# Performance work log

Measured on AMD Instinct MI355X. Metric: run time of the kernel, lower is better.

## Reference

```python
import jax, jax.numpy as jnp
import numpy as np

N_HEADS = 16
MAX_LEN = 4096
D_MODEL = 1024
EPS = 1e-6


def setup_inputs() -> dict:
    key = jax.random.key(0)
    ks = jax.random.split(key, 12)
    B, L, D = 4, 4096, D_MODEL
    s = 1.0 / np.sqrt(D)
    inp = {
        "q": jax.random.normal(ks[0], (B, L, D), jnp.float32),
        "k": jax.random.normal(ks[1], (B, L, D), jnp.float32),
        "v": jax.random.normal(ks[2], (B, L, D), jnp.float32),
        "Wq": jax.random.normal(ks[3], (D, D), jnp.float32) * s,
        "bq": jax.random.normal(ks[4], (D,), jnp.float32) * s,
        "Wk": jax.random.normal(ks[5], (D, D), jnp.float32) * s,
        "bk": jax.random.normal(ks[6], (D,), jnp.float32) * s,
        "Wv": jax.random.normal(ks[7], (D, D), jnp.float32) * s,
        "bv": jax.random.normal(ks[8], (D,), jnp.float32) * s,
        "Wo": jax.random.normal(ks[9], (D, D), jnp.float32) * s,
        "bo": jax.random.normal(ks[10], (D,), jnp.float32) * s,
    }
    return inp


def _cos_attn(q, k, v, Wq, bq, Wk, bk, Wv, bv, Wo, bo):
    B, Lq, D = q.shape
    Lk = k.shape[1]
    H = N_HEADS
    hd = D // H
    # torch Linear: x @ W^T + b
    qh = (q @ Wq.T + bq).reshape(B, Lq, H, hd).transpose(0, 2, 1, 3)  # b h l d
    kh = (k @ Wk.T + bk).reshape(B, Lk, H, hd).transpose(0, 2, 1, 3)
    vh = (v @ Wv.T + bv).reshape(B, Lk, H, hd).transpose(0, 2, 1, 3)
    qh = jax.nn.relu(qh)
    kh = jax.nn.relu(kh)
    # weight_index buffer: pi*(1..max_len)/(2*max_len), shape (1,1,L,1)
    idx = (np.pi * jnp.arange(1, MAX_LEN + 1, dtype=jnp.float32) / (2 * MAX_LEN))
    qi = idx[:Lq][None, None, :, None]
    ki = idx[:Lk][None, None, :, None]
    q_ = jnp.concatenate([qh * jnp.sin(qi), qh * jnp.cos(qi)], axis=-1)  # b h l 2d
    k_ = jnp.concatenate([kh * jnp.sin(ki), kh * jnp.cos(ki)], axis=-1)
    kv_ = jnp.einsum("bnld,bnlm->bndm", k_, vh)  # b h 2d d
    z_ = 1.0 / jnp.maximum(jnp.einsum("bnld,bnd->bnl", q_, jnp.sum(k_, axis=2)), EPS)
    attn = jnp.einsum("bnld,bndm,bnl->bnlm", q_, kv_, z_)  # b h l d
    attn = attn.transpose(0, 2, 1, 3).reshape(B, Lq, D)
    return attn @ Wo.T + bo  # dropout: eval mode (identity)


def reference(q, k, v, Wq, bq, Wk, bk, Wv, bv, Wo, bo):
    return _cos_attn(q, k, v, Wq, bq, Wk, bk, Wv, bv, Wo, bo)
```

## Files before the change

### kernel.cpp

```cpp
#include <hip/hip_runtime.h>

typedef __bf16 bf16x8 __attribute__((ext_vector_type(8)));
typedef float f32x4 __attribute__((ext_vector_type(4)));

#define PI_F 3.14159265358979323846f

__device__ __forceinline__ unsigned short f2bf(float f) {
  unsigned u = __builtin_bit_cast(unsigned, f);
  u += 0x7fffu + ((u >> 16) & 1u);
  return (unsigned short)(u >> 16);
}

__device__ __forceinline__ unsigned scale_pair(unsigned w, float f) {
  const float lo = __builtin_bit_cast(float, w << 16);
  const float hi = __builtin_bit_cast(float, w & 0xffff0000u);
  return (unsigned)f2bf(lo * f) | ((unsigned)f2bf(hi * f) << 16);
}

#define GLD16(gp, lp)                                          \
  __builtin_amdgcn_global_load_lds(                            \
      (const __attribute__((address_space(1))) void*)(gp),     \
      (__attribute__((address_space(3))) void*)(lp), 16, 0, 0)

struct AReg { float4 a0, a1, a2, a3, a4, a5, a6, a7; };

__device__ __forceinline__ uint4 cvtpk16(float4 x, float4 y) {
  unsigned c0, c1, c2, c3;
  asm("v_cvt_pk_bf16_f32 %0, %1, %2" : "=v"(c0) : "v"(x.x), "v"(x.y));
  asm("v_cvt_pk_bf16_f32 %0, %1, %2" : "=v"(c1) : "v"(x.z), "v"(x.w));
  asm("v_cvt_pk_bf16_f32 %0, %1, %2" : "=v"(c2) : "v"(y.x), "v"(y.y));
  asm("v_cvt_pk_bf16_f32 %0, %1, %2" : "=v"(c3) : "v"(y.z), "v"(y.w));
  uint4 u; u.x = c0; u.y = c1; u.z = c2; u.w = c3;
  return u;
}

__device__ __forceinline__ uint2 cvtpk8(float a, float b, float c, float d) {
  unsigned lo, hi;
  asm("v_cvt_pk_bf16_f32 %0, %1, %2" : "=v"(lo) : "v"(a), "v"(b));
  asm("v_cvt_pk_bf16_f32 %0, %1, %2" : "=v"(hi) : "v"(c), "v"(d));
  uint2 r; r.x = lo; r.y = hi;
  return r;
}

__device__ __forceinline__ void unpack8(uint4 w, float* f) {
  f[0] = __builtin_bit_cast(float, w.x << 16);
  f[1] = __builtin_bit_cast(float, w.x & 0xffff0000u);
  f[2] = __builtin_bit_cast(float, w.y << 16);
  f[3] = __builtin_bit_cast(float, w.y & 0xffff0000u);
  f[4] = __builtin_bit_cast(float, w.z << 16);
  f[5] = __builtin_bit_cast(float, w.z & 0xffff0000u);
  f[6] = __builtin_bit_cast(float, w.w << 16);
  f[7] = __builtin_bit_cast(float, w.w & 0xffff0000u);
}

__global__ __launch_bounds__(256) void convert_w(
    const float* __restrict__ Wq, const float* __restrict__ Wk,
    const float* __restrict__ Wv, const float* __restrict__ Wo,
    unsigned short* __restrict__ Wqb, unsigned short* __restrict__ Wkb,
    unsigned short* __restrict__ Wvb, unsigned short* __restrict__ Wob) {
  const int region = blockIdx.y;
  const float* s; unsigned short* d;
  switch (region) {
    case 0: s = Wq; d = Wqb; break;
    case 1: s = Wk; d = Wkb; break;
    case 2: s = Wv; d = Wvb; break;
    default: s = Wo; d = Wob; break;
  }
  const float4* s4 = (const float4*)s;
  ushort4* d4 = (ushort4*)d;
  const int n4 = 262144;
  for (int i = blockIdx.x * 256 + threadIdx.x; i < n4; i += gridDim.x * 256) {
    float4 f = s4[i];
    ushort4 o;
    o.x = f2bf(f.x); o.y = f2bf(f.y); o.z = f2bf(f.z); o.w = f2bf(f.w);
    d4[i] = o;
  }
}

template <int MODE, bool AF32>
__global__ __launch_bounds__(512, 2) void gemm256(
    const void* __restrict__ Ain, const unsigned short* __restrict__ Bw,
    const float* __restrict__ bias, void* __restrict__ out) {
  constexpr int K = 1024, NKT = 16;
  __shared__ unsigned short S[65536];
  const int tid = threadIdx.x;
  const int wave = tid >> 6, lane = tid & 63;
  const int fr = lane & 15, fq = lane >> 4;
  const int wr = wave >> 2, wc = wave & 3;
  const int cpx = gridDim.x >> 3;
  const int wg = (blockIdx.x & 7) * cpx + (blockIdx.x >> 3);
  const int mt = wg >> 2, ntile = wg & 3;
  const int m0 = mt * 256, n0 = ntile * 256;

  const int srow = tid >> 3;
  const int ac16 = tid & 7;
  const int scolE = ((ac16 << 4) ^ ((srow & 7) << 4)) >> 1;
  const unsigned short* bSrc = Bw + (size_t)(n0 + srow) * K + scolE;
  const unsigned short* aSrcB =
      AF32 ? (const unsigned short*)nullptr
           : ((const unsigned short*)Ain + (size_t)(m0 + srow) * K + scolE);
  const float* A32 = (const float*)Ain;
  const int awoff = (ac16 ^ (srow & 7)) << 3;
  AReg R;

#define BSTAGE(kt_, buf_) do {                                                     \
    const int kc_ = (kt_) * 64;                                                    \
    GLD16(bSrc + kc_,                  S + (buf_) * 32768 + 16384 + wave * 512);   \
    GLD16(bSrc + (size_t)65536 + kc_,  S + (buf_) * 32768 + 20480 + wave * 512);   \
    GLD16(bSrc + (size_t)131072 + kc_, S + (buf_) * 32768 + 24576 + wave * 512);   \
    GLD16(bSrc + (size_t)196608 + kc_, S + (buf_) * 32768 + 28672 + wave * 512);   \
  } while (0)

#define ASTAGE(kt_, buf_) do {                                                     \
    const int kc_ = (kt_) * 64;                                                    \
    GLD16(aSrcB + kc_,                  S + (buf_) * 32768 +     0 + wave * 512);  \
    GLD16(aSrcB + (size_t)65536 + kc_,  S + (buf_) * 32768 +  4096 + wave * 512);  \
    GLD16(aSrcB + (size_t)131072 + kc_, S + (buf_) * 32768 +  8192 + wave * 512);  \
    GLD16(aSrcB + (size_t)196608 + kc_, S + (buf_) * 32768 + 12288 + wave * 512);  \
  } while (0)

#define ALOAD_ALL(kt_) do {                                                        \
    const int kc_ = (kt_) * 64;                                                    \
    const float4* p_;                                                              \
    p_ = (const float4*)(A32 + (size_t)(m0 + srow) * K + kc_) + ac16 * 2;          \
    R.a0 = p_[0]; R.a1 = p_[1];                                                    \
    p_ = (const float4*)(A32 + (size_t)(m0 + 64 + srow) * K + kc_) + ac16 * 2;     \
    R.a2 = p_[0]; R.a3 = p_[1];                                                    \
    p_ = (const float4*)(A32 + (size_t)(m0 + 128 + srow) * K + kc_) + ac16 * 2;    \
    R.a4 = p_[0]; R.a5 = p_[1];                                                    \
    p_ = (const float4*)(A32 + (size_t)(m0 + 192 + srow) * K + kc_) + ac16 * 2;    \
    R.a6 = p_[0]; R.a7 = p_[1];                                                    \
  } while (0)

#define AWRITE_ALL(buf_) do {                                                      \
    unsigned short* dst_ = &S[(buf_) * 32768 + srow * 64 + awoff];                 \
    *(uint4*)(dst_)         = cvtpk16(R.a0, R.a1);                                 \
    *(uint4*)(dst_ + 4096)  = cvtpk16(R.a2, R.a3);                                 \
    *(uint4*)(dst_ + 8192)  = cvtpk16(R.a4, R.a5);                                 \
    *(uint4*)(dst_ + 12288) = cvtpk16(R.a6, R.a7);                                 \
  } while (0)

  const int xorv = (fr & 7) << 4;
  const unsigned cbE0 = (unsigned)(((fq * 16) ^ xorv) >> 1);
  const unsigned cbE1 = (unsigned)(((64 + fq * 16) ^ xorv) >> 1);

  f32x4 acc[8][4] = {};
  if constexpr (AF32) {
    ALOAD_ALL(0);
    BSTAGE(0, 0);
    AWRITE_ALL(0);
  } else {
    BSTAGE(0, 0);
    ASTAGE(0, 0);
  }
  asm volatile("s_waitcnt vmcnt(0) lgkmcnt(0)" ::: "memory");
  __syncthreads();

  for (int kt = 0; kt < NKT; ++kt) {
    const int buf = kt & 1;
    const unsigned aB = (unsigned)(buf * 32768 + wr * 8192 + fr * 64);
    const unsigned bB = (unsigned)(buf * 32768 + 16384 + (wc >> 1) * 8192 +
                                   ((wc & 1) * 64 + fr) * 64);
#pragma unroll
    for (int ph = 0; ph < 4; ++ph) {
      const int mh = ph >> 1, nh = ph & 1;
      bf16x8 af[4][2], bfr[2][2];
#pragma unroll
      for (int mm = 0; mm < 4; ++mm) {
        const unsigned r = aB + (unsigned)((mh * 4 + mm) * 1024);
        af[mm][0] = *(const bf16x8*)&S[r + cbE0];
        af[mm][1] = *(const bf16x8*)&S[r + cbE1];
      }
#pragma unroll
      for (int nn = 0; nn < 2; ++nn) {
        const unsigned r = bB + (unsigned)((nh * 2 + nn) * 1024);
        bfr[nn][0] = *(const bf16x8*)&S[r + cbE0];
        bfr[nn][1] = *(const bf16x8*)&S[r + cbE1];
      }
      if (ph == 0 && kt + 1 < NKT) {
        if constexpr (AF32) ALOAD_ALL(kt + 1);
        BSTAGE(kt + 1, buf ^ 1);
        if constexpr (!AF32) ASTAGE(kt + 1, buf ^ 1);
      }
      if constexpr (AF32) {
        if (ph == 2 && kt + 1 < NKT) AWRITE_ALL(buf ^ 1);
      }
      __builtin_amdgcn_s_barrier();
      __builtin_amdgcn_s_setprio(1);
#pragma unroll
      for (int mm = 0; mm < 4; ++mm)
#pragma unroll
        for (int nn = 0; nn < 2; ++nn) {
          acc[mh * 4 + mm][nh * 2 + nn] = __builtin_amdgcn_mfma_f32_16x16x32_bf16(
              af[mm][0], bfr[nn][0], acc[mh * 4 + mm][nh * 2 + nn], 0, 0, 0);
          acc[mh * 4 + mm][nh * 2 + nn] = __builtin_amdgcn_mfma_f32_16x16x32_bf16(
              af[mm][1], bfr[nn][1], acc[mh * 4 + mm][nh * 2 + nn], 0, 0, 0);
        }
      __builtin_amdgcn_s_setprio(0);
      if (ph == 3) {
        if constexpr (AF32) {
          asm volatile("s_waitcnt lgkmcnt(0)" ::: "memory");
          __builtin_amdgcn_sched_barrier(0);
        }
        asm volatile("s_waitcnt vmcnt(0)" ::: "memory");
      }
      __builtin_amdgcn_s_barrier();
    }
  }
#undef BSTAGE
#undef ASTAGE
#undef ALOAD_ALL
#undef AWRITE_ALL

  const int rowb = m0 + wr * 128 + fq * 4;
  const int colb = n0 + wc * 64 + fr;
  const int rtb0 = wr * 128 + fq * 4;
  const int mlo = m0 & 4095;
  const int b16 = (m0 >> 12) << 4;
  const int hbase = n0 >> 6;

  if constexpr (MODE == 0) {
#pragma unroll
    for (int nq = 0; nq < 4; ++nq) {
      const int col = colb + nq * 16;
      const float bb = bias[col];
      const int h = col >> 6, dd = col & 63;
#pragma unroll
      for (int mq = 0; mq < 8; ++mq) {
#pragma unroll
        for (int rr = 0; rr < 4; ++rr) {
          const int i = rowb + mq * 16 + rr;
          const int b = i >> 12, l = i & 4095;
          const float val = fmaxf(acc[mq][nq][rr] + bb, 0.0f);
          ((unsigned short*)out)[((size_t)((b << 4) + h) * 4096 + l) * 64 + dd] = f2bf(val);
        }
      }
    }
  } else if constexpr (MODE == 2) {
    float* Sf = (float*)S;
    float* O = (float*)out;
    float bb4[4];
#pragma unroll
    for (int nq = 0; nq < 4; ++nq) bb4[nq] = bias[colb + nq * 16];
    const int colL = wc * 64;
#pragma unroll
    for (int h4 = 0; h4 < 4; ++h4) {
      __syncthreads();
      if (wr == (h4 >> 1)) {
        const int mqb = (h4 & 1) * 4;
#pragma unroll
        for (int mq2 = 0; mq2 < 4; ++mq2) {
          const int rl = mq2 * 16 + fq * 4;
#pragma unroll
          for (int nq = 0; nq < 4; ++nq) {
#pragma unroll
            for (int rr = 0; rr < 4; ++rr)
              Sf[(rl + rr) * 260 + colL + nq * 16 + fr] = acc[mqb + mq2][nq][rr] + bb4[nq];
          }
        }
      }
      __syncthreads();
#pragma unroll
      for (int i = 0; i < 8; ++i) {
        const int rl = wave * 8 + i;
        const int gr = m0 + h4 * 64 + rl;
        f32x4 v4 = *(const f32x4*)&Sf[rl * 260 + lane * 4];
        __builtin_nontemporal_store(v4, (f32x4*)(O + (size_t)gr * 1024 + n0 + lane * 4));
      }
    }
  } else {
    float bb4[4];
#pragma unroll
    for (int nq = 0; nq < 4; ++nq) bb4[nq] = bias[colb + nq * 16];
#pragma unroll
    for (int mq = 0; mq < 8; ++mq)
#pragma unroll
      for (int nq = 0; nq < 4; ++nq)
#pragma unroll
        for (int rr = 0; rr < 4; ++rr) {
          float val = acc[mq][nq][rr] + bb4[nq];
          if constexpr (MODE == 5) val = fmaxf(val, 0.0f);
          acc[mq][nq][rr] = val;
        }
    unsigned short* G = (unsigned short*)out;
    __syncthreads();
#pragma unroll
    for (int mq = 0; mq < 8; ++mq) {
      const int rtb = rtb0 + mq * 16;
#pragma unroll
      for (int nq = 0; nq < 4; ++nq) {
        const int ct = wc * 64 + nq * 16 + fr;
        uint2 w = cvtpk8(acc[mq][nq][0], acc[mq][nq][1], acc[mq][nq][2], acc[mq][nq][3]);
        *(uint2*)&S[ct * 256 + (rtb ^ ((ct & 7) << 2))] = w;
      }
    }
    __syncthreads();
#pragma unroll
    for (int it = 0; it < 16; ++it) {
      const int ct = it * 16 + (tid >> 5);
      const int lo = (tid & 31) << 3;
      const int sw = (ct & 7) << 2;
      uint2 r0 = *(const uint2*)&S[ct * 256 + (lo ^ sw)];
      uint2 r1 = *(const uint2*)&S[ct * 256 + ((lo + 4) ^ sw)];
      uint4 w; w.x = r0.x; w.y = r0.y; w.z = r1.x; w.w = r1.y;
      const int h = hbase + (ct >> 6), dd = ct & 63;
      const size_t addr = ((size_t)(b16 + h) * 64 + dd) * 4096 + mlo + lo;
      *(uint4*)(G + addr) = w;
    }
  }
}

__global__ __launch_bounds__(256, 2) void kv_gemm(
    const unsigned short* __restrict__ Vt,
    const unsigned short* __restrict__ Kt,
    float* __restrict__ kvp) {
  __shared__ unsigned short As[64 * 64];
  __shared__ unsigned short Bs[128 * 64];
  __shared__ float sn[512], cn[512];
  const int tid = threadIdx.x, wave = tid >> 6, lane = tid & 63;
  const int fr = lane & 15, fq = lane >> 4;
  const int ls = blockIdx.x, bh = blockIdx.y;
  const size_t base = (size_t)bh * 64 * 4096;
  {
    float s0, c0, s1, c1;
    __sincosf(PI_F * (float)(ls * 512 + tid + 1) * (1.0f / 8192.0f), &s0, &c0);
    __sincosf(PI_F * (float)(ls * 512 + tid + 257) * (1.0f / 8192.0f), &s1, &c1);
    sn[tid] = s0; cn[tid] = c0;
    sn[tid + 256] = s1; cn[tid + 256] = c1;
  }
  f32x4 acc[5][2] = {};
  bf16x8 ones;
#pragma unroll
  for (int j = 0; j < 8; ++j) ones[j] = (__bf16)1.0f;
  for (int t = 0; t < 8; ++t) {
    const int l0 = ls * 512 + t * 64;
    __syncthreads();
#pragma unroll
    for (int j = 0; j < 2; ++j) {
      const int p = j * 256 + tid;
      const int row = p >> 3, cc = (p & 7) ^ (row & 7);
      GLD16(Vt + base + (size_t)row * 4096 + l0 + cc * 8,
            As + ((j << 8) + (wave << 6)) * 8);
    }
#pragma unroll
    for (int j = 0; j < 2; ++j) {
      const int p = j * 256 + tid;
      const int kr = p >> 3, cc = p & 7;
      const uint4 w = *(const uint4*)(Kt + base + (size_t)kr * 4096 + l0 + cc * 8);
      const int tl = t * 64 + cc * 8;
      float kf[8];
      unpack8(w, kf);
      const float4 sA = *(const float4*)&sn[tl], sB = *(const float4*)&sn[tl + 4];
      const float4 cA = *(const float4*)&cn[tl], cB = *(const float4*)&cn[tl + 4];
      float4 x0, x1;
      x0.x = kf[0] * sA.x; x0.y = kf[1] * sA.y; x0.z = kf[2] * sA.z; x0.w = kf[3] * sA.w;
      x1.x = kf[4] * sB.x; x1.y = kf[5] * sB.y; x1.z = kf[6] * sB.z; x1.w = kf[7] * sB.w;
      const uint4 wsn = cvtpk16(x0, x1);
      x0.x = kf[0] * cA.x; x0.y = kf[1] * cA.y; x0.z = kf[2] * cA.z; x0.w = kf[3] * cA.w;
      x1.x = kf[4] * cB.x; x1.y = kf[5] * cB.y; x1.z = kf[6] * cB.z; x1.w = kf[7] * cB.w;
      const uint4 wcn = cvtpk16(x0, x1);
      const int sw_ = cc ^ (kr & 7);
      *(uint4*)&Bs[(kr * 8 + sw_) * 8] = wsn;
      *(uint4*)&Bs[((kr + 64) * 8 + sw_) * 8] = wcn;
    }
    __syncthreads();
#pragma unroll
    for (int kk = 0; kk < 2; ++kk) {
      const int ch = kk * 4 + fq;
      bf16x8 a[4], b[2];
#pragma unroll
      for (int m = 0; m < 4; ++m) {
        const int r = m * 16 + fr;
        a[m] = *(const bf16x8*)&As[(r * 8 + (ch ^ (r & 7))) * 8];
      }
#pragma unroll
      for (int n = 0; n < 2; ++n) {
        const int r = wave * 32 + n * 16 + fr;
        b[n] = *(const bf16x8*)&Bs[(r * 8 + (ch ^ (r & 7))) * 8];
      }
#pragma unroll
      for (int m = 0; m < 4; ++m)
#pragma unroll
        for (int n = 0; n < 2; ++n)
          acc[m][n] = __builtin_amdgcn_mfma_f32_16x16x32_bf16(a[m], b[n], acc[m][n], 0, 0, 0);
#pragma unroll
      for (int n = 0; n < 2; ++n)
        acc[4][n] = __builtin_amdgcn_mfma_f32_16x16x32_bf16(ones, b[n], acc[4][n], 0, 0, 0);
    }
  }
  float* outp = kvp + ((size_t)bh * 8 + ls) * (65 * 128);
  const int colb = wave * 32 + fr;
#pragma unroll
  for (int n = 0; n < 2; ++n) {
    const int col = colb + n * 16;
#pragma unroll
    for (int m = 0; m < 4; ++m)
#pragma unroll
      for (int r = 0; r < 4; ++r)
        outp[(m * 16 + fq * 4 + r) * 128 + col] = acc[m][n][r];
    if (fq == 0) outp[64 * 128 + col] = acc[4][n][0];
  }
}

__global__ __launch_bounds__(256) void kv_reduce(
    const float* __restrict__ kvp, unsigned short* __restrict__ kv_ext) {
  const int bh = blockIdx.x;
  for (int e = threadIdx.x; e < 80 * 128; e += 256) {
    const int row = e >> 7, c = e & 127;
    float v = 0.0f;
    if (row < 65) {
#pragma unroll
      for (int ls = 0; ls < 8; ++ls)
        v += kvp[((size_t)bh * 8 + ls) * (65 * 128) + row * 128 + c];
    }
    kv_ext[(size_t)bh * (80 * 128) + e] = f2bf(v);
  }
}

__global__ __launch_bounds__(256) void attn_phase2(
    const unsigned short* __restrict__ Qh, const unsigned short* __restrict__ kve,
    unsigned short* __restrict__ attn) {
  __shared__ unsigned short Qs[128 * 128];
  __shared__ unsigned short Ws[80 * 128];
  const int tid = threadIdx.x, wave = tid >> 6, lane = tid & 63;
  const int fr = lane & 15, fq = lane >> 4;
  const int l0 = blockIdx.x * 128;
  const int bh = blockIdx.y, b = bh >> 4, h = bh & 15;
#pragma unroll
  for (int j = 0; j < 5; ++j) {
    const int p = j * 256 + tid;
    const int r = p >> 4, scn = p & 15;
    const int cc = scn ^ (r & 7);
    GLD16(kve + ((size_t)bh * 80 + r) * 128 + cc * 8,
          Ws + ((size_t)(j * 256 + wave * 64)) * 8);
  }
#pragma unroll
  for (int it = 0; it < 4; ++it) {
    const int qc = it * 256 + tid;
    const int r = qc >> 3, dc = qc & 7;
    const uint4 w = *(const uint4*)(Qh + ((size_t)bh * 4096 + l0 + r) * 64 + dc * 8);
    float sv, cv;
    __sincosf(PI_F * (float)(l0 + r + 1) * (1.0f / 8192.0f), &sv, &cv);
    uint4 osn, ocs;
    osn.x = scale_pair(w.x, sv); osn.y = scale_pair(w.y, sv);
    osn.z = scale_pair(w.z, sv); osn.w = scale_pair(w.w, sv);
    ocs.x = scale_pair(w.x, cv); ocs.y = scale_pair(w.y, cv);
    ocs.z = scale_pair(w.z, cv); ocs.w = scale_pair(w.w, cv);
    const int ps = r * 16 + (dc ^ (r & 7));
    *(uint4*)&Qs[ps * 8] = osn;
    *(uint4*)&Qs[(ps + 8) * 8] = ocs;
  }
  __syncthreads();
  f32x4 acc[2][5] = {};
#pragma unroll
  for (int kk = 0; kk < 4; ++kk) {
    const int cc = kk * 4 + fq;
    bf16x8 a[2], bb[5];
#pragma unroll
    for (int m = 0; m < 2; ++m) {
      const int r = wave * 32 + m * 16 + fr;
      a[m] = *(const bf16x8*)&Qs[(r * 16 + (cc ^ (r & 7))) * 8];
    }
#pragma unroll
    for (int n = 0; n < 5; ++n) {
      const int r = n * 16 + fr;
      bb[n] = *(const bf16x8*)&Ws[(r * 16 + (cc ^ (r & 7))) * 8];
    }
#pragma unroll
    for (int m = 0; m < 2; ++m)
#pragma unroll
      for (int n = 0; n < 5; ++n)
        acc[m][n] = __builtin_amdgcn_mfma_f32_16x16x32_bf16(a[m], bb[n], acc[m][n], 0, 0, 0);
  }
#pragma unroll
  for (int m = 0; m < 2; ++m) {
#pragma unroll
    for (int r = 0; r < 4; ++r) {
      const float den = __shfl(acc[m][4][r], lane & 48);
      const float z = 1.0f / fmaxf(den, 1e-6f);
      const int l = l0 + wave * 32 + m * 16 + fq * 4 + r;
      const size_t ro = ((size_t)b * 4096 + l) * 1024 + (size_t)h * 64;
#pragma unroll
      for (int n = 0; n < 4; ++n)
        attn[ro + n * 16 + fr] = f2bf(acc[m][n][r] * z);
    }
  }
}

extern "C" void kernel_launch(void* const* d_in, const int* in_sizes, int n_in,
                              void* d_out, int out_size, void* d_ws, size_t ws_size,
                              hipStream_t stream) {
  (void)in_sizes; (void)n_in; (void)out_size; (void)ws_size;
  const float* q  = (const float*)d_in[0];
  const float* k  = (const float*)d_in[1];
  const float* v  = (const float*)d_in[2];
  const float* Wq = (const float*)d_in[3];
  const float* bq = (const float*)d_in[4];
  const float* Wk = (const float*)d_in[5];
  const float* bk = (const float*)d_in[6];
  const float* Wv = (const float*)d_in[7];
  const float* bvp = (const float*)d_in[8];
  const float* Wo = (const float*)d_in[9];
  const float* bo = (const float*)d_in[10];

  char* ws = (char*)d_ws;
  unsigned short* Wqb = (unsigned short*)(ws + 0);
  unsigned short* Wkb = (unsigned short*)(ws + 2097152);
  unsigned short* Wvb = (unsigned short*)(ws + 4194304);
  unsigned short* Wob = (unsigned short*)(ws + 6291456);
  unsigned short* Qh  = (unsigned short*)(ws + 8388608);
  unsigned short* Vt  = (unsigned short*)(ws + 41943040);
  unsigned short* Kt  = (unsigned short*)(ws + 75497472);
  unsigned short* attnb = Kt;
  float* kvp          = (float*)(ws + 109051904);
  unsigned short* kve = (unsigned short*)(ws + 126091264);

  convert_w<<<dim3(128, 4), 256, 0, stream>>>(Wq, Wk, Wv, Wo, Wqb, Wkb, Wvb, Wob);
  gemm256<0, true><<<256, 512, 0, stream>>>(q, Wqb, bq, Qh);
  gemm256<5, true><<<256, 512, 0, stream>>>(k, Wkb, bk, Kt);
  gemm256<4, true><<<256, 512, 0, stream>>>(v, Wvb, bvp, Vt);
  kv_gemm<<<dim3(8, 64), 256, 0, stream>>>(Vt, Kt, kvp);
  kv_reduce<<<64, 256, 0, stream>>>(kvp, kve);
  attn_phase2<<<dim3(32, 64), 256, 0, stream>>>(Qh, kve, attnb);
  gemm256<2, false><<<256, 512, 0, stream>>>(attnb, Wob, bo, (float*)d_out);
}
```

Baseline: 279.8 us.

## Restructure GEMM main loop from four phases into two with B fragment reuse

Replaces the four-phase inner k-step (each reloading A and B fragments from LDS) with two halves. B fragments are loaded once per k-tile and reused across both M halves, which halves the barriers per tile and cuts LDS reads of B. The final output store also switches from a nontemporal store to a regular store. Holding both B halves raises register pressure, and the change alters how prefetch and LDS writes interleave with the MFMA work.

```diff
diff --git a/kernel.cpp b/kernel.cpp
--- a/kernel.cpp
+++ b/kernel.cpp
@@ -161,51 +161,69 @@
     const unsigned aB = (unsigned)(buf * 32768 + wr * 8192 + fr * 64);
     const unsigned bB = (unsigned)(buf * 32768 + 16384 + (wc >> 1) * 8192 +
                                    ((wc & 1) * 64 + fr) * 64);
-#pragma unroll
-    for (int ph = 0; ph < 4; ++ph) {
-      const int mh = ph >> 1, nh = ph & 1;
-      bf16x8 af[4][2], bfr[2][2];
-#pragma unroll
-      for (int mm = 0; mm < 4; ++mm) {
-        const unsigned r = aB + (unsigned)((mh * 4 + mm) * 1024);
-        af[mm][0] = *(const bf16x8*)&S[r + cbE0];
-        af[mm][1] = *(const bf16x8*)&S[r + cbE1];
-      }
+    bf16x8 af[4][2], b0[2][2], b1[2][2];
+#pragma unroll
+    for (int mm = 0; mm < 4; ++mm) {
+      const unsigned r = aB + (unsigned)(mm * 1024);
+      af[mm][0] = *(const bf16x8*)&S[r + cbE0];
+      af[mm][1] = *(const bf16x8*)&S[r + cbE1];
+    }
+#pragma unroll
+    for (int nn = 0; nn < 2; ++nn) {
+      const unsigned r0 = bB + (unsigned)(nn * 1024);
+      b0[nn][0] = *(const bf16x8*)&S[r0 + cbE0];
+      b0[nn][1] = *(const bf16x8*)&S[r0 + cbE1];
+      const unsigned r1 = bB + (unsigned)((2 + nn) * 1024);
+      b1[nn][0] = *(const bf16x8*)&S[r1 + cbE0];
+      b1[nn][1] = *(const bf16x8*)&S[r1 + cbE1];
+    }
+    if (kt + 1 < NKT) {
+      if constexpr (AF32) {
+        ALOAD_ALL(kt + 1);
+        BSTAGE(kt + 1, buf ^ 1);
+      } else {
+        BSTAGE(kt + 1, buf ^ 1);
+        ASTAGE(kt + 1, buf ^ 1);
+      }
+    }
+    __builtin_amdgcn_s_barrier();
+    __builtin_amdgcn_s_setprio(1);
+#pragma unroll
+    for (int mm = 0; mm < 4; ++mm) {
 #pragma unroll
       for (int nn = 0; nn < 2; ++nn) {
-        const unsigned r = bB + (unsigned)((nh * 2 + nn) * 1024);
-        bfr[nn][0] = *(const bf16x8*)&S[r + cbE0];
-        bfr[nn][1] = *(const bf16x8*)&S[r + cbE1];
-      }
-      if (ph == 0 && kt + 1 < NKT) {
-        if constexpr (AF32) ALOAD_ALL(kt + 1);
-        BSTAGE(kt + 1, buf ^ 1);
-        if constexpr (!AF32) ASTAGE(kt + 1, buf ^ 1);
-      }
-      if constexpr (AF32) {
-        if (ph == 2 && kt + 1 < NKT) AWRITE_ALL(buf ^ 1);
-      }
-      __builtin_amdgcn_s_barrier();
-      __builtin_amdgcn_s_setprio(1);
-#pragma unroll
-      for (int mm = 0; mm < 4; ++mm)
-#pragma unroll
-        for (int nn = 0; nn < 2; ++nn) {
-          acc[mh * 4 + mm][nh * 2 + nn] = __builtin_amdgcn_mfma_f32_16x16x32_bf16(
-              af[mm][0], bfr[nn][0], acc[mh * 4 + mm][nh * 2 + nn], 0, 0, 0);
-          acc[mh * 4 + mm][nh * 2 + nn] = __builtin_amdgcn_mfma_f32_16x16x32_bf16(
-              af[mm][1], bfr[nn][1], acc[mh * 4 + mm][nh * 2 + nn], 0, 0, 0);
-        }
-      __builtin_amdgcn_s_setprio(0);
-      if (ph == 3) {
-        if constexpr (AF32) {
-          asm volatile("s_waitcnt lgkmcnt(0)" ::: "memory");
-          __builtin_amdgcn_sched_barrier(0);
-        }
-        asm volatile("s_waitcnt vmcnt(0)" ::: "memory");
-      }
-      __builtin_amdgcn_s_barrier();
-    }
+        acc[mm][nn] = __builtin_amdgcn_mfma_f32_16x16x32_bf16(af[mm][0], b0[nn][0], acc[mm][nn], 0, 0, 0);
+        acc[mm][nn] = __builtin_amdgcn_mfma_f32_16x16x32_bf16(af[mm][1], b0[nn][1], acc[mm][nn], 0, 0, 0);
+        acc[mm][2 + nn] = __builtin_amdgcn_mfma_f32_16x16x32_bf16(af[mm][0], b1[nn][0], acc[mm][2 + nn], 0, 0, 0);
+        acc[mm][2 + nn] = __builtin_amdgcn_mfma_f32_16x16x32_bf16(af[mm][1], b1[nn][1], acc[mm][2 + nn], 0, 0, 0);
+      }
+    }
+    __builtin_amdgcn_s_setprio(0);
+    __builtin_amdgcn_s_barrier();
+#pragma unroll
+    for (int mm = 0; mm < 4; ++mm) {
+      const unsigned r = aB + (unsigned)((4 + mm) * 1024);
+      af[mm][0] = *(const bf16x8*)&S[r + cbE0];
+      af[mm][1] = *(const bf16x8*)&S[r + cbE1];
+    }
+    if constexpr (AF32) {
+      if (kt + 1 < NKT) AWRITE_ALL(buf ^ 1);
+    }
+    __builtin_amdgcn_s_barrier();
+    __builtin_amdgcn_s_setprio(1);
+#pragma unroll
+    for (int mm = 0; mm < 4; ++mm) {
+#pragma unroll
+      for (int nn = 0; nn < 2; ++nn) {
+        acc[4 + mm][nn] = __builtin_amdgcn_mfma_f32_16x16x32_bf16(af[mm][0], b0[nn][0], acc[4 + mm][nn], 0, 0, 0);
+        acc[4 + mm][nn] = __builtin_amdgcn_mfma_f32_16x16x32_bf16(af[mm][1], b0[nn][1], acc[4 + mm][nn], 0, 0, 0);
+        acc[4 + mm][2 + nn] = __builtin_amdgcn_mfma_f32_16x16x32_bf16(af[mm][0], b1[nn][0], acc[4 + mm][2 + nn], 0, 0, 0);
+        acc[4 + mm][2 + nn] = __builtin_amdgcn_mfma_f32_16x16x32_bf16(af[mm][1], b1[nn][1], acc[4 + mm][2 + nn], 0, 0, 0);
+      }
+    }
+    __builtin_amdgcn_s_setprio(0);
+    asm volatile("s_waitcnt vmcnt(0) lgkmcnt(0)" ::: "memory");
+    __builtin_amdgcn_s_barrier();
   }
 #undef BSTAGE
 #undef ASTAGE
@@ -265,7 +283,7 @@
         const int rl = wave * 8 + i;
         const int gr = m0 + h4 * 64 + rl;
         f32x4 v4 = *(const f32x4*)&Sf[rl * 260 + lane * 4];
-        __builtin_nontemporal_store(v4, (f32x4*)(O + (size_t)gr * 1024 + n0 + lane * 4));
+        *(f32x4*)(O + (size_t)gr * 1024 + n0 + lane * 4) = v4;
       }
     }
   } else {
```

Result: faster. 262.5 us (-6.2%).

## Shrink projection GEMM tiles to 128x128 with 4-deep B-operand pipeline

Applied to the files above, without the earlier changes.

Replaces the 256x256-tile, 512-thread GEMM with a 128x128-tile, 256-thread kernel using K-step 32 and a 4-stage LDS ring for async global-to-LDS loads. The grid grows from 256 to 1024 blocks, which fills more CUs on a 256-CU part and cuts shared memory per block so more blocks can be resident. The epilogues are reworked for the smaller tile. In exchange, arithmetic intensity per tile drops, each input is re-read from global memory more often, and there are more barriers per unit of work.

```diff
diff --git a/kernel.cpp b/kernel.cpp
--- a/kernel.cpp
+++ b/kernel.cpp
@@ -21,8 +21,6 @@
   __builtin_amdgcn_global_load_lds(                            \
       (const __attribute__((address_space(1))) void*)(gp),     \
       (__attribute__((address_space(3))) void*)(lp), 16, 0, 0)
-
-struct AReg { float4 a0, a1, a2, a3, a4, a5, a6, a7; };
 
 __device__ __forceinline__ uint4 cvtpk16(float4 x, float4 y) {
   unsigned c0, c1, c2, c3;
@@ -78,143 +76,127 @@
 }
 
 template <int MODE, bool AF32>
-__global__ __launch_bounds__(512, 2) void gemm256(
+__global__ __launch_bounds__(256, AF32 ? 3 : 2) void gemm128(
     const void* __restrict__ Ain, const unsigned short* __restrict__ Bw,
     const float* __restrict__ bias, void* __restrict__ out) {
-  constexpr int K = 1024, NKT = 16;
-  __shared__ unsigned short S[65536];
+  constexpr int K = 1024, NKT = 32;
+  __shared__ unsigned short S[AF32 ? 24576 : 32768];
+  constexpr int BOFF = AF32 ? 8192 : 16384;
   const int tid = threadIdx.x;
   const int wave = tid >> 6, lane = tid & 63;
   const int fr = lane & 15, fq = lane >> 4;
-  const int wr = wave >> 2, wc = wave & 3;
-  const int cpx = gridDim.x >> 3;
-  const int wg = (blockIdx.x & 7) * cpx + (blockIdx.x >> 3);
-  const int mt = wg >> 2, ntile = wg & 3;
-  const int m0 = mt * 256, n0 = ntile * 256;
-
-  const int srow = tid >> 3;
-  const int ac16 = tid & 7;
-  const int scolE = ((ac16 << 4) ^ ((srow & 7) << 4)) >> 1;
-  const unsigned short* bSrc = Bw + (size_t)(n0 + srow) * K + scolE;
-  const unsigned short* aSrcB =
+  const int wr = wave >> 1, wc = wave & 1;
+  const int wg = (blockIdx.x & 7) * 128 + (blockIdx.x >> 3);
+  const int mt = wg >> 3, nt = wg & 7;
+  const int m0 = mt * 128, n0 = nt * 128;
+
+  const int crow = tid >> 2, cq = tid & 3;
+  const int colE = ((cq ^ ((crow >> 1) & 3)) << 3);
+  const unsigned short* bSrc0 = Bw + (size_t)(n0 + crow) * K + colE;
+  const unsigned short* bSrc1 = bSrc0 + (size_t)64 * K;
+  const unsigned short* aSrc0 =
       AF32 ? (const unsigned short*)nullptr
-           : ((const unsigned short*)Ain + (size_t)(m0 + srow) * K + scolE);
+           : ((const unsigned short*)Ain + (size_t)(m0 + crow) * K + colE);
+  const unsigned short* aSrc1 = AF32 ? (const unsigned short*)nullptr : aSrc0 + (size_t)64 * K;
   const float* A32 = (const float*)Ain;
-  const int awoff = (ac16 ^ (srow & 7)) << 3;
-  AReg R;
-
-#define BSTAGE(kt_, buf_) do {                                                     \
-    const int kc_ = (kt_) * 64;                                                    \
-    GLD16(bSrc + kc_,                  S + (buf_) * 32768 + 16384 + wave * 512);   \
-    GLD16(bSrc + (size_t)65536 + kc_,  S + (buf_) * 32768 + 20480 + wave * 512);   \
-    GLD16(bSrc + (size_t)131072 + kc_, S + (buf_) * 32768 + 24576 + wave * 512);   \
-    GLD16(bSrc + (size_t)196608 + kc_, S + (buf_) * 32768 + 28672 + wave * 512);   \
+  const int arow = tid >> 1, ah = tid & 1;
+  const int ac0 = (((ah * 2) ^ ((arow >> 1) & 3)) << 3);
+  const int ac1 = (((ah * 2 + 1) ^ ((arow >> 1) & 3)) << 3);
+  const float* aSrc32_0 = A32 + (size_t)(m0 + arow) * K + ac0;
+  const float* aSrc32_1 = A32 + (size_t)(m0 + arow) * K + ac1;
+  float4 R0, R1, R2, R3;
+
+#define BSTAGE(kt_) do {                                                        \
+    const int kc_ = (kt_) * 32, bo_ = BOFF + ((kt_) & 3) * 4096;                \
+    GLD16(bSrc0 + kc_, S + bo_ + wave * 512);                                   \
+    GLD16(bSrc1 + kc_, S + bo_ + 2048 + wave * 512);                            \
   } while (0)
 
-#define ASTAGE(kt_, buf_) do {                                                     \
-    const int kc_ = (kt_) * 64;                                                    \
-    GLD16(aSrcB + kc_,                  S + (buf_) * 32768 +     0 + wave * 512);  \
-    GLD16(aSrcB + (size_t)65536 + kc_,  S + (buf_) * 32768 +  4096 + wave * 512);  \
-    GLD16(aSrcB + (size_t)131072 + kc_, S + (buf_) * 32768 +  8192 + wave * 512);  \
-    GLD16(aSrcB + (size_t)196608 + kc_, S + (buf_) * 32768 + 12288 + wave * 512);  \
+#define ASTAGE(kt_) do {                                                        \
+    const int kc_ = (kt_) * 32, ao_ = ((kt_) & 3) * 4096;                       \
+    GLD16(aSrc0 + kc_, S + ao_ + wave * 512);                                   \
+    GLD16(aSrc1 + kc_, S + ao_ + 2048 + wave * 512);                            \
   } while (0)
 
-#define ALOAD_ALL(kt_) do {                                                        \
-    const int kc_ = (kt_) * 64;                                                    \
-    const float4* p_;                                                              \
-    p_ = (const float4*)(A32 + (size_t)(m0 + srow) * K + kc_) + ac16 * 2;          \
-    R.a0 = p_[0]; R.a1 = p_[1];                                                    \
-    p_ = (const float4*)(A32 + (size_t)(m0 + 64 + srow) * K + kc_) + ac16 * 2;     \
-    R.a2 = p_[0]; R.a3 = p_[1];                                                    \
-    p_ = (const float4*)(A32 + (size_t)(m0 + 128 + srow) * K + kc_) + ac16 * 2;    \
-    R.a4 = p_[0]; R.a5 = p_[1];                                                    \
-    p_ = (const float4*)(A32 + (size_t)(m0 + 192 + srow) * K + kc_) + ac16 * 2;    \
-    R.a6 = p_[0]; R.a7 = p_[1];                                                    \
+#define ALOAD(kt_) do {                                                         \
+    const int kc_ = (kt_) * 32;                                                 \
+    R0 = *(const float4*)(aSrc32_0 + kc_);                                      \
+    R1 = *(const float4*)(aSrc32_0 + kc_ + 4);                                  \
+    R2 = *(const float4*)(aSrc32_1 + kc_);                                      \
+    R3 = *(const float4*)(aSrc32_1 + kc_ + 4);                                  \
   } while (0)
 
-#define AWRITE_ALL(buf_) do {                                                      \
-    unsigned short* dst_ = &S[(buf_) * 32768 + srow * 64 + awoff];                 \
-    *(uint4*)(dst_)         = cvtpk16(R.a0, R.a1);                                 \
-    *(uint4*)(dst_ + 4096)  = cvtpk16(R.a2, R.a3);                                 \
-    *(uint4*)(dst_ + 8192)  = cvtpk16(R.a4, R.a5);                                 \
-    *(uint4*)(dst_ + 12288) = cvtpk16(R.a6, R.a7);                                 \
+#define AWRITE(kt_) do {                                                        \
+    unsigned short* d_ = &S[((kt_) & 1) * 4096 + arow * 32];                    \
+    *(uint4*)(d_ + ah * 16)     = cvtpk16(R0, R1);                              \
+    *(uint4*)(d_ + ah * 16 + 8) = cvtpk16(R2, R3);                              \
   } while (0)
 
-  const int xorv = (fr & 7) << 4;
-  const unsigned cbE0 = (unsigned)(((fq * 16) ^ xorv) >> 1);
-  const unsigned cbE1 = (unsigned)(((64 + fq * 16) ^ xorv) >> 1);
-
-  f32x4 acc[8][4] = {};
+  const unsigned fcol = (unsigned)((fq ^ ((fr >> 1) & 3)) << 3);
+
+  f32x4 acc[4][4] = {};
   if constexpr (AF32) {
-    ALOAD_ALL(0);
-    BSTAGE(0, 0);
-    AWRITE_ALL(0);
+    BSTAGE(0);
+    ALOAD(0);
+    BSTAGE(1);
+    BSTAGE(2);
+    AWRITE(0);
+    asm volatile("s_waitcnt lgkmcnt(0)" ::: "memory");
+    __syncthreads();
   } else {
-    BSTAGE(0, 0);
-    ASTAGE(0, 0);
-  }
-  asm volatile("s_waitcnt vmcnt(0) lgkmcnt(0)" ::: "memory");
-  __syncthreads();
+    ASTAGE(0); BSTAGE(0);
+    ASTAGE(1); BSTAGE(1);
+    ASTAGE(2); BSTAGE(2);
+    asm volatile("s_waitcnt vmcnt(8)" ::: "memory");
+    __syncthreads();
+  }
 
   for (int kt = 0; kt < NKT; ++kt) {
-    const int buf = kt & 1;
-    const unsigned aB = (unsigned)(buf * 32768 + wr * 8192 + fr * 64);
-    const unsigned bB = (unsigned)(buf * 32768 + 16384 + (wc >> 1) * 8192 +
-                                   ((wc & 1) * 64 + fr) * 64);
-#pragma unroll
-    for (int ph = 0; ph < 4; ++ph) {
-      const int mh = ph >> 1, nh = ph & 1;
-      bf16x8 af[4][2], bfr[2][2];
-#pragma unroll
-      for (int mm = 0; mm < 4; ++mm) {
-        const unsigned r = aB + (unsigned)((mh * 4 + mm) * 1024);
-        af[mm][0] = *(const bf16x8*)&S[r + cbE0];
-        af[mm][1] = *(const bf16x8*)&S[r + cbE1];
-      }
-#pragma unroll
-      for (int nn = 0; nn < 2; ++nn) {
-        const unsigned r = bB + (unsigned)((nh * 2 + nn) * 1024);
-        bfr[nn][0] = *(const bf16x8*)&S[r + cbE0];
-        bfr[nn][1] = *(const bf16x8*)&S[r + cbE1];
-      }
-      if (ph == 0 && kt + 1 < NKT) {
-        if constexpr (AF32) ALOAD_ALL(kt + 1);
-        BSTAGE(kt + 1, buf ^ 1);
-        if constexpr (!AF32) ASTAGE(kt + 1, buf ^ 1);
-      }
-      if constexpr (AF32) {
-        if (ph == 2 && kt + 1 < NKT) AWRITE_ALL(buf ^ 1);
-      }
-      __builtin_amdgcn_s_barrier();
-      __builtin_amdgcn_s_setprio(1);
-#pragma unroll
-      for (int mm = 0; mm < 4; ++mm)
-#pragma unroll
-        for (int nn = 0; nn < 2; ++nn) {
-          acc[mh * 4 + mm][nh * 2 + nn] = __builtin_amdgcn_mfma_f32_16x16x32_bf16(
-              af[mm][0], bfr[nn][0], acc[mh * 4 + mm][nh * 2 + nn], 0, 0, 0);
-          acc[mh * 4 + mm][nh * 2 + nn] = __builtin_amdgcn_mfma_f32_16x16x32_bf16(
-              af[mm][1], bfr[nn][1], acc[mh * 4 + mm][nh * 2 + nn], 0, 0, 0);
-        }
-      __builtin_amdgcn_s_setprio(0);
-      if (ph == 3) {
-        if constexpr (AF32) {
-          asm volatile("s_waitcnt lgkmcnt(0)" ::: "memory");
-          __builtin_amdgcn_sched_barrier(0);
-        }
+    const unsigned abuf = (unsigned)((AF32 ? (kt & 1) : (kt & 3)) * 4096);
+    const unsigned bbuf = (unsigned)(BOFF + (kt & 3) * 4096);
+    bf16x8 a[4], b[4];
+#pragma unroll
+    for (int m = 0; m < 4; ++m) {
+      const unsigned row = (unsigned)(wr * 64 + m * 16 + fr);
+      a[m] = *(const bf16x8*)&S[abuf + row * 32 + fcol];
+    }
+#pragma unroll
+    for (int n = 0; n < 4; ++n) {
+      const unsigned row = (unsigned)(wc * 64 + n * 16 + fr);
+      b[n] = *(const bf16x8*)&S[bbuf + row * 32 + fcol];
+    }
+    if constexpr (AF32) {
+      if (kt + 1 < NKT) ALOAD(kt + 1);
+      if (kt + 3 < NKT) BSTAGE(kt + 3);
+    } else {
+      if (kt + 3 < NKT) { ASTAGE(kt + 3); BSTAGE(kt + 3); }
+    }
+    __builtin_amdgcn_s_setprio(1);
+#pragma unroll
+    for (int m = 0; m < 4; ++m)
+#pragma unroll
+      for (int n = 0; n < 4; ++n)
+        acc[m][n] = __builtin_amdgcn_mfma_f32_16x16x32_bf16(a[m], b[n], acc[m][n], 0, 0, 0);
+    __builtin_amdgcn_s_setprio(0);
+    if constexpr (AF32) {
+      if (kt + 1 < NKT) AWRITE(kt + 1);
+      asm volatile("s_waitcnt lgkmcnt(0)" ::: "memory");
+    } else {
+      if (kt < NKT - 3) {
+        asm volatile("s_waitcnt vmcnt(8)" ::: "memory");
+      } else {
         asm volatile("s_waitcnt vmcnt(0)" ::: "memory");
       }
-      __builtin_amdgcn_s_barrier();
-    }
+    }
+    __builtin_amdgcn_s_barrier();
   }
 #undef BSTAGE
 #undef ASTAGE
-#undef ALOAD_ALL
-#undef AWRITE_ALL
-
-  const int rowb = m0 + wr * 128 + fq * 4;
+#undef ALOAD
+#undef AWRITE
+
+  const int rowb = m0 + wr * 64 + fq * 4;
   const int colb = n0 + wc * 64 + fr;
-  const int rtb0 = wr * 128 + fq * 4;
   const int mlo = m0 & 4095;
   const int b16 = (m0 >> 12) << 4;
   const int hbase = n0 >> 6;
@@ -226,7 +208,7 @@
       const float bb = bias[col];
       const int h = col >> 6, dd = col & 63;
 #pragma unroll
-      for (int mq = 0; mq < 8; ++mq) {
+      for (int mq = 0; mq < 4; ++mq) {
 #pragma unroll
         for (int rr = 0; rr < 4; ++rr) {
           const int i = rowb + mq * 16 + rr;
@@ -242,30 +224,29 @@
     float bb4[4];
 #pragma unroll
     for (int nq = 0; nq < 4; ++nq) bb4[nq] = bias[colb + nq * 16];
-    const int colL = wc * 64;
-#pragma unroll
-    for (int h4 = 0; h4 < 4; ++h4) {
+#pragma unroll
+    for (int p = 0; p < 2; ++p) {
       __syncthreads();
-      if (wr == (h4 >> 1)) {
-        const int mqb = (h4 & 1) * 4;
-#pragma unroll
-        for (int mq2 = 0; mq2 < 4; ++mq2) {
-          const int rl = mq2 * 16 + fq * 4;
+      if (wr == p) {
+#pragma unroll
+        for (int mq = 0; mq < 4; ++mq) {
 #pragma unroll
           for (int nq = 0; nq < 4; ++nq) {
 #pragma unroll
-            for (int rr = 0; rr < 4; ++rr)
-              Sf[(rl + rr) * 260 + colL + nq * 16 + fr] = acc[mqb + mq2][nq][rr] + bb4[nq];
+            for (int rr = 0; rr < 4; ++rr) {
+              const int rl = mq * 16 + fq * 4 + rr;
+              Sf[rl * 132 + wc * 64 + nq * 16 + fr] = acc[mq][nq][rr] + bb4[nq];
+            }
           }
         }
       }
       __syncthreads();
 #pragma unroll
-      for (int i = 0; i < 8; ++i) {
-        const int rl = wave * 8 + i;
-        const int gr = m0 + h4 * 64 + rl;
-        f32x4 v4 = *(const f32x4*)&Sf[rl * 260 + lane * 4];
-        __builtin_nontemporal_store(v4, (f32x4*)(O + (size_t)gr * 1024 + n0 + lane * 4));
+      for (int it = 0; it < 8; ++it) {
+        const int rl = it * 8 + (tid >> 5);
+        const int col = (tid & 31) << 2;
+        f32x4 v4 = *(const f32x4*)&Sf[rl * 132 + col];
+        *(f32x4*)(O + (size_t)(m0 + p * 64 + rl) * 1024 + n0 + col) = v4;
       }
     }
   } else {
@@ -273,7 +254,7 @@
 #pragma unroll
     for (int nq = 0; nq < 4; ++nq) bb4[nq] = bias[colb + nq * 16];
 #pragma unroll
-    for (int mq = 0; mq < 8; ++mq)
+    for (int mq = 0; mq < 4; ++mq)
 #pragma unroll
       for (int nq = 0; nq < 4; ++nq)
 #pragma unroll
@@ -283,29 +264,34 @@
           acc[mq][nq][rr] = val;
         }
     unsigned short* G = (unsigned short*)out;
-    __syncthreads();
-#pragma unroll
-    for (int mq = 0; mq < 8; ++mq) {
-      const int rtb = rtb0 + mq * 16;
-#pragma unroll
-      for (int nq = 0; nq < 4; ++nq) {
-        const int ct = wc * 64 + nq * 16 + fr;
-        uint2 w = cvtpk8(acc[mq][nq][0], acc[mq][nq][1], acc[mq][nq][2], acc[mq][nq][3]);
-        *(uint2*)&S[ct * 256 + (rtb ^ ((ct & 7) << 2))] = w;
-      }
-    }
-    __syncthreads();
-#pragma unroll
-    for (int it = 0; it < 16; ++it) {
-      const int ct = it * 16 + (tid >> 5);
-      const int lo = (tid & 31) << 3;
-      const int sw = (ct & 7) << 2;
-      uint2 r0 = *(const uint2*)&S[ct * 256 + (lo ^ sw)];
-      uint2 r1 = *(const uint2*)&S[ct * 256 + ((lo + 4) ^ sw)];
-      uint4 w; w.x = r0.x; w.y = r0.y; w.z = r1.x; w.w = r1.y;
-      const int h = hbase + (ct >> 6), dd = ct & 63;
-      const size_t addr = ((size_t)(b16 + h) * 64 + dd) * 4096 + mlo + lo;
-      *(uint4*)(G + addr) = w;
+    const int rtb0 = wr * 64 + fq * 4;
+#pragma unroll
+    for (int p = 0; p < 2; ++p) {
+      __syncthreads();
+      if (wc == p) {
+#pragma unroll
+        for (int mq = 0; mq < 4; ++mq) {
+          const int rtb = rtb0 + mq * 16;
+#pragma unroll
+          for (int nq = 0; nq < 4; ++nq) {
+            const int ctl = nq * 16 + fr;
+            uint2 w = cvtpk8(acc[mq][nq][0], acc[mq][nq][1], acc[mq][nq][2], acc[mq][nq][3]);
+            *(uint2*)&S[ctl * 128 + (rtb ^ ((ctl & 7) << 2))] = w;
+          }
+        }
+      }
+      __syncthreads();
+#pragma unroll
+      for (int it = 0; it < 4; ++it) {
+        const int ctl = it * 16 + (tid >> 4);
+        const int lo = (tid & 15) << 3;
+        const int sw = (ctl & 7) << 2;
+        uint2 r0 = *(const uint2*)&S[ctl * 128 + (lo ^ sw)];
+        uint2 r1 = *(const uint2*)&S[ctl * 128 + ((lo + 4) ^ sw)];
+        uint4 w; w.x = r0.x; w.y = r0.y; w.z = r1.x; w.w = r1.y;
+        const size_t addr = ((size_t)(b16 + hbase + p) * 64 + ctl) * 4096 + mlo + lo;
+        *(uint4*)(G + addr) = w;
+      }
     }
   }
 }
@@ -516,11 +502,11 @@
   unsigned short* kve = (unsigned short*)(ws + 126091264);
 
   convert_w<<<dim3(128, 4), 256, 0, stream>>>(Wq, Wk, Wv, Wo, Wqb, Wkb, Wvb, Wob);
-  gemm256<0, true><<<256, 512, 0, stream>>>(q, Wqb, bq, Qh);
-  gemm256<5, true><<<256, 512, 0, stream>>>(k, Wkb, bk, Kt);
-  gemm256<4, true><<<256, 512, 0, stream>>>(v, Wvb, bvp, Vt);
+  gemm128<0, true><<<1024, 256, 0, stream>>>(q, Wqb, bq, Qh);
+  gemm128<5, true><<<1024, 256, 0, stream>>>(k, Wkb, bk, Kt);
+  gemm128<4, true><<<1024, 256, 0, stream>>>(v, Wvb, bvp, Vt);
   kv_gemm<<<dim3(8, 64), 256, 0, stream>>>(Vt, Kt, kvp);
   kv_reduce<<<64, 256, 0, stream>>>(kvp, kve);
   attn_phase2<<<dim3(32, 64), 256, 0, stream>>>(Qh, kve, attnb);
-  gemm256<2, false><<<256, 512, 0, stream>>>(attnb, Wob, bo, (float*)d_out);
-}
+  gemm128<2, false><<<1024, 256, 0, stream>>>(attnb, Wob, bo, (float*)d_out);
+}
```

After: 359.5 us. 28.5% more time.
